# Performance work log

Measured on AMD Instinct MI355X. Metric: run time of the kernel, lower is better.

The kernel has to match this reference:

```python
import math
import jax, jax.numpy as jnp
import numpy as np

B, C, T = 2, 512, 2048
HEADS, NFREQS, NDECAY = 8, 4, 4
HD = C // HEADS  # head dim = 64


def _conv1x1(x, W, b):
    # pointwise Conv1d: W [out, in], b [out], x [B, in, T]
    return jnp.einsum('oi,bit->bot', W, x) + b[:, None]


def setup_inputs() -> dict:
    key = jax.random.key(0)
    ks = jax.random.split(key, 12)
    s = 1.0 / math.sqrt(C)
    inp = {
        'x': jax.random.normal(ks[0], (B, C, T), jnp.float32),
        'Wq': jax.random.normal(ks[1], (C, C), jnp.float32) * s,
        'bq': jnp.zeros((C,), jnp.float32),
        'Wk': jax.random.normal(ks[2], (C, C), jnp.float32) * s,
        'bk': jnp.zeros((C,), jnp.float32),
        'Wc': jax.random.normal(ks[3], (C, C), jnp.float32) * s,
        'bc': jnp.zeros((C,), jnp.float32),
        'Wqf': jax.random.normal(ks[4], (HEADS * NFREQS, C), jnp.float32) * s,
        'bqf': jnp.zeros((HEADS * NFREQS,), jnp.float32),
        # query_decay init: weight *= 0.01, bias = -2 (as in the torch module)
        'Wqd': jax.random.normal(ks[5], (HEADS * NDECAY, C), jnp.float32) * (s * 0.01),
        'bqd': jnp.full((HEADS * NDECAY,), -2.0, jnp.float32),
        'Wp': jax.random.normal(ks[6], (C, C), jnp.float32) * s,
        'bp': jnp.zeros((C,), jnp.float32),
    }
    return inp


def reference(x, Wq, bq, Wk, bk, Wc, bc, Wqf, bqf, Wqd, bqd, Wp, bp):
    Bx, Cx, Tx = x.shape
    idx = jnp.arange(Tx, dtype=x.dtype)
    delta = idx[:, None] - idx[None, :]  # [T, T]

    queries = _conv1x1(x, Wq, bq).reshape(Bx, HEADS, HD, Tx)
    keys = _conv1x1(x, Wk, bk).reshape(Bx, HEADS, HD, Tx)
    dots = jnp.einsum('bhct,bhcs->bhts', keys, queries) / math.sqrt(HD)

    # frequency bias
    periods = jnp.arange(1, NFREQS + 1, dtype=x.dtype)
    freq_kernel = jnp.cos(2 * math.pi * delta / periods[:, None, None])  # [f, T, T]
    freq_q = _conv1x1(x, Wqf, bqf).reshape(Bx, HEADS, NFREQS, Tx) / math.sqrt(NFREQS)
    dots = dots + jnp.einsum('fts,bhfs->bhts', freq_kernel, freq_q)

    # decay bias
    decays = jnp.arange(1, NDECAY + 1, dtype=x.dtype)
    decay_q = jax.nn.sigmoid(_conv1x1(x, Wqd, bqd).reshape(Bx, HEADS, NDECAY, Tx)) / 2
    decay_kernel = -decays[:, None, None] * jnp.abs(delta) / math.sqrt(NDECAY)
    dots = dots + jnp.einsum('fts,bhfs->bhts', decay_kernel, decay_q)

    # mask self-attention diagonal with -100, softmax over keys axis (t, dim=2)
    eye = jnp.eye(Tx, dtype=bool)
    dots = jnp.where(eye[None, None], jnp.asarray(-100.0, x.dtype), dots)
    weights = jax.nn.softmax(dots, axis=2)

    content = _conv1x1(x, Wc, bc).reshape(Bx, HEADS, HD, Tx)
    result = jnp.einsum('bhts,bhct->bhcs', weights, content).reshape(Bx, Cx, Tx)
    return x + _conv1x1(result, Wp, bp)
```

## Files before the change

kernel.cpp:

```cpp
#include <hip/hip_runtime.h>
#include <math.h>

#define T_SEQ 2048
#define C_DIM 512
#define B_SZ  2
#define NHEAD 8
#define HD    64
#define DP    128
#define MTOT  1600
#define NTILE 32

typedef unsigned short u16t;
typedef unsigned int   u32t;
typedef float f32x4 __attribute__((ext_vector_type(4)));
typedef short s16x8 __attribute__((ext_vector_type(8)));

__device__ __forceinline__ u32t pack2(float a, float b) {
    u32t r;
    asm("v_cvt_pk_bf16_f32 %0, %1, %2" : "=v"(r) : "v"(a), "v"(b));
    return r;
}
__device__ __forceinline__ u16t f2bf(float f) {
    union { float f; u32t u; } v; v.f = f;
    u32t r = v.u + 0x7fffu + ((v.u >> 16) & 1u);
    return (u16t)(r >> 16);
}
__device__ __forceinline__ float bf2f(u16t h) {
    union { u32t u; float f; } v; v.u = (u32t)h << 16; return v.f;
}

#define GLD16(g, l) __builtin_amdgcn_global_load_lds( \
    (const __attribute__((address_space(1))) u32t*)(g), \
    (__attribute__((address_space(3))) u32t*)(l), 16, 0, 0)

__global__ __launch_bounds__(256)
void wconv_kernel(const float* __restrict__ Wq, const float* __restrict__ Wk,
                  const float* __restrict__ Wc, const float* __restrict__ Wqf,
                  const float* __restrict__ Wqd, const float* __restrict__ Wp,
                  const float* __restrict__ bq, const float* __restrict__ bk,
                  const float* __restrict__ bc, const float* __restrict__ bqf,
                  const float* __restrict__ bqd,
                  u16t* __restrict__ Wcat, u16t* __restrict__ Wpbf,
                  float* __restrict__ biascat)
{
    int r = blockIdx.x, tid = threadIdx.x;
    if (r < MTOT) {
        const float* src;
        if (r < 512) src = Wq + (long long)r * C_DIM;
        else if (r < 1024) src = Wk + (long long)(r - 512) * C_DIM;
        else if (r < 1536) src = Wc + (long long)(r - 1024) * C_DIM;
        else if (r < 1568) src = Wqf + (long long)(r - 1536) * C_DIM;
        else src = Wqd + (long long)(r - 1568) * C_DIM;
        float2 v = *(const float2*)(src + tid * 2);
        *(u32t*)(Wcat + (long long)r * C_DIM + tid * 2) = pack2(v.x, v.y);
    } else if (r < MTOT + 512) {
        int rr = r - MTOT;
        float2 v = *(const float2*)(Wp + (long long)rr * C_DIM + tid * 2);
        *(u32t*)(Wpbf + (long long)rr * C_DIM + tid * 2) = pack2(v.x, v.y);
    } else {
        for (int i = tid; i < MTOT; i += 256) {
            float bv;
            if (i < 512) bv = bq[i];
            else if (i < 1024) bv = bk[i - 512];
            else if (i < 1536) bv = bc[i - 1024];
            else if (i < 1568) bv = bqf[i - 1536];
            else bv = bqd[i - 1568];
            biascat[i] = bv;
        }
    }
}

__global__ __launch_bounds__(256)
void xt_kernel(const float* __restrict__ x, u16t* __restrict__ xT)
{
    __shared__ float tile[64][65];
    int b = blockIdx.z, c0 = blockIdx.y * 64, t0 = blockIdx.x * 64;
    int tid = threadIdx.x;
    const float* xb = x + ((long long)b * C_DIM + c0) * T_SEQ + t0;
#pragma unroll
    for (int rr = 0; rr < 16; ++rr) {
        int row = rr * 4 + (tid >> 6);
        tile[row][tid & 63] = xb[(long long)row * T_SEQ + (tid & 63)];
    }
    __syncthreads();
    int tt = tid >> 2, cs = (tid & 3) * 16;
    u32t ov[8];
#pragma unroll
    for (int u = 0; u < 8; ++u)
        ov[u] = pack2(tile[cs + u * 2][tt], tile[cs + u * 2 + 1][tt]);
    u16t* dst = xT + ((long long)b * T_SEQ + t0 + tt) * C_DIM + c0 + cs;
    *(uint4*)(dst) = make_uint4(ov[0], ov[1], ov[2], ov[3]);
    *(uint4*)(dst + 8) = make_uint4(ov[4], ov[5], ov[6], ov[7]);
}

template<int BM, int BN, int MODE>
__global__ __launch_bounds__(256)
void gemm_big(const u16t* __restrict__ A, const u16t* __restrict__ Bm,
              const float* __restrict__ biasv, const float* __restrict__ x,
              u16t* __restrict__ Qbf, u16t* __restrict__ Kbf,
              u16t* __restrict__ Vbf, float* __restrict__ fqd,
              float* __restrict__ outp)
{
    constexpr int WM = BM / 2, WN = BN / 2, MT = WM / 16, NT = WN / 16;
    __shared__ u16t At[2][BM * 64];
    __shared__ u16t Bt[2][BN * 64];
    int b = blockIdx.z, m0 = blockIdx.y * BM, n0 = blockIdx.x * BN;
    int tid = threadIdx.x, w = tid >> 6, lane = tid & 63;
    int wy = w >> 1, wx = w & 1;
    int l16 = lane & 15, l4 = lane >> 4;
    const u16t* Bb = Bm + (long long)b * T_SEQ * C_DIM;

    auto stage = [&](int kt, int bufi) {
        int k0 = kt * 64;
#pragma unroll
        for (int i = 0; i < BM / 32; ++i) {
            int rb = (w * (BM / 32) + i) * 8;
            int row = rb + (lane >> 3);
            int c = (lane & 7) ^ (row & 7);
            GLD16(A + (long long)(m0 + row) * C_DIM + k0 + c * 8, &At[bufi][rb * 64]);
        }
#pragma unroll
        for (int i = 0; i < BN / 32; ++i) {
            int rb = (w * (BN / 32) + i) * 8;
            int row = rb + (lane >> 3);
            int c = (lane & 7) ^ (row & 7);
            GLD16(Bb + (long long)(n0 + row) * C_DIM + k0 + c * 8, &Bt[bufi][rb * 64]);
        }
    };

    f32x4 acc[MT][NT] = {};
    stage(0, 0);
    for (int kt = 0; kt < 8; ++kt) {
        __syncthreads();
        if (kt < 7) stage(kt + 1, (kt + 1) & 1);
        const u16t* Ab = At[kt & 1];
        const u16t* Bb2 = Bt[kt & 1];
#pragma unroll
        for (int kb = 0; kb < 2; ++kb) {
            int co = ((kb * 4 + l4) ^ (l16 & 7)) * 8;
            s16x8 bf[NT], af[MT];
#pragma unroll
            for (int nt = 0; nt < NT; ++nt)
                bf[nt] = *(const s16x8*)(&Bb2[(wx * WN + nt * 16 + l16) * 64 + co]);
#pragma unroll
            for (int mt = 0; mt < MT; ++mt)
                af[mt] = *(const s16x8*)(&Ab[(wy * WM + mt * 16 + l16) * 64 + co]);
            __builtin_amdgcn_s_setprio(1);
#pragma unroll
            for (int mt = 0; mt < MT; ++mt)
#pragma unroll
                for (int nt = 0; nt < NT; ++nt)
                    acc[mt][nt] = __builtin_amdgcn_mfma_f32_16x16x32_bf16(
                        af[mt], bf[nt], acc[mt][nt], 0, 0, 0);
            __builtin_amdgcn_s_setprio(0);
        }
    }

    if (MODE == 0) {
        int my = blockIdx.y;
        if (my < 8) {
            bool isQ = my < 4;
            float sc = isQ ? 0.125f : 1.0f;
#pragma unroll
            for (int nt = 0; nt < NT; ++nt) {
                int n = n0 + wx * WN + nt * 16 + l16;
#pragma unroll
                for (int mt = 0; mt < MT; ++mt) {
                    int m = m0 + wy * WM + mt * 16 + l4 * 4;
                    int idx = isQ ? m : m - 512;
                    int h = idx >> 6, d0 = idx & 63;
                    u16t* dst = (isQ ? Qbf : Kbf) +
                        ((long long)(b * NHEAD + h) * T_SEQ + n) * DP + d0;
                    float v0 = sc * (acc[mt][nt][0] + biasv[m + 0]);
                    float v1 = sc * (acc[mt][nt][1] + biasv[m + 1]);
                    float v2 = sc * (acc[mt][nt][2] + biasv[m + 2]);
                    float v3 = sc * (acc[mt][nt][3] + biasv[m + 3]);
                    *(uint2*)dst = make_uint2(pack2(v0, v1), pack2(v2, v3));
                }
            }
        } else if (my < 12) {
#pragma unroll
            for (int nt = 0; nt < NT; ++nt) {
                int n = n0 + wx * WN + nt * 16 + l16;
#pragma unroll
                for (int mt = 0; mt < MT; ++mt)
#pragma unroll
                    for (int j = 0; j < 4; ++j) {
                        int m = m0 + wy * WM + mt * 16 + l4 * 4 + j;
                        int c = m - 1024;
                        Vbf[((long long)b * C_DIM + c) * T_SEQ + n] =
                            f2bf(acc[mt][nt][j] + biasv[m]);
                    }
            }
        } else {
#pragma unroll
            for (int nt = 0; nt < NT; ++nt) {
                int n = n0 + wx * WN + nt * 16 + l16;
#pragma unroll
                for (int mt = 0; mt < MT; ++mt)
#pragma unroll
                    for (int j = 0; j < 4; ++j) {
                        int m = m0 + wy * WM + mt * 16 + l4 * 4 + j;
                        int r = m - 1536;
                        if (r < 64)
                            fqd[((long long)b * 64 + r) * T_SEQ + n] =
                                acc[mt][nt][j] + biasv[m];
                    }
            }
        }
    } else {
#pragma unroll
        for (int nt = 0; nt < NT; ++nt) {
            int n = n0 + wx * WN + nt * 16 + l16;
#pragma unroll
            for (int mt = 0; mt < MT; ++mt)
#pragma unroll
                for (int j = 0; j < 4; ++j) {
                    int m = m0 + wy * WM + mt * 16 + l4 * 4 + j;
                    long long o = ((long long)b * C_DIM + m) * T_SEQ + n;
                    outp[o] = acc[mt][nt][j] + biasv[m] + x[o];
                }
        }
    }
}

__global__ __launch_bounds__(256)
void ext_kernel(const float* __restrict__ fqd, u16t* __restrict__ Qbf,
                u16t* __restrict__ Kbf, float* __restrict__ dcoef)
{
    int s = blockIdx.x * 256 + threadIdx.x;
    int bh = blockIdx.y, b = bh >> 3, h = bh & 7;
    const float* base = fqd + (long long)b * 64 * T_SEQ;
    float dsum = 0.f;
    u32t eq[4], ek[4];
#pragma unroll
    for (int f = 0; f < 4; ++f) {
        float fq = base[(long long)(h * 4 + f) * T_SEQ + s] * 0.5f;
        float zd = base[(long long)(32 + h * 4 + f) * T_SEQ + s];
        dsum += (float)(f + 1) / (1.f + __expf(-zd));
        float a = 2.0f * (float)s / (float)(f + 1);
        float cv = cospif(a), sv = sinpif(a);
        ek[f] = pack2(cv, sv);
        eq[f] = pack2(fq * cv, fq * sv);
    }
    uint4 z = make_uint4(0, 0, 0, 0);
    u16t* qrow = Qbf + ((long long)bh * T_SEQ + s) * DP;
    *(uint4*)(qrow + 64) = make_uint4(eq[0], eq[1], eq[2], eq[3]);
#pragma unroll
    for (int i = 0; i < 7; ++i) *(uint4*)(qrow + 72 + i * 8) = z;
    u16t* krow = Kbf + ((long long)bh * T_SEQ + s) * DP;
    *(uint4*)(krow + 64) = make_uint4(ek[0], ek[1], ek[2], ek[3]);
#pragma unroll
    for (int i = 0; i < 7; ++i) *(uint4*)(krow + 72 + i * 8) = z;
    dcoef[(long long)bh * T_SEQ + s] = 0.25f * dsum;
}

__global__ __launch_bounds__(256)
void knorm_kernel(const u16t* __restrict__ Kbf, float* __restrict__ knorm)
{
    __shared__ float wmax[4];
    int tile = blockIdx.x, bh = blockIdx.y, tid = threadIdx.x;
    int row = tid >> 2, part = tid & 3;
    const u16t* rp = Kbf + ((long long)bh * T_SEQ + tile * 64 + row) * DP + part * 16;
    float ss = 0.f;
#pragma unroll
    for (int i = 0; i < 2; ++i) {
        s16x8 v = *(const s16x8*)(rp + i * 8);
#pragma unroll
        for (int e = 0; e < 8; ++e) { float f = bf2f((u16t)v[e]); ss += f * f; }
    }
    ss += __shfl_xor(ss, 1, 64);
    ss += __shfl_xor(ss, 2, 64);
    float nrm = sqrtf(ss + 4.1f);
#pragma unroll
    for (int off = 4; off < 64; off <<= 1) nrm = fmaxf(nrm, __shfl_xor(nrm, off, 64));
    if ((tid & 63) == 0) wmax[tid >> 6] = nrm;
    __syncthreads();
    if (tid == 0)
        knorm[bh * NTILE + tile] =
            fmaxf(fmaxf(wmax[0], wmax[1]), fmaxf(wmax[2], wmax[3]));
}

__global__ __launch_bounds__(256)
void attn_kernel(const u16t* __restrict__ Qbf, const u16t* __restrict__ Kbf,
                 const u16t* __restrict__ Vbf, const float* __restrict__ dcoef,
                 const float* __restrict__ knorm, u16t* __restrict__ Rt)
{
    __shared__ u16t Kt[2][64 * DP];
    __shared__ u16t Vt[2][64 * 64];
    __shared__ u16t Pl[4][16 * 64];
    __shared__ u32t voteLds[4];

    int bh = blockIdx.y, b = bh >> 3, h = bh & 7;
    int j0 = blockIdx.x;
    int s0 = j0 * 64;
    int tid = threadIdx.x, w = tid >> 6, lane = tid & 63;
    int l16 = lane & 15, l4 = lane >> 4;
    const u16t* Qg = Qbf + (long long)bh * T_SEQ * DP;
    const u16t* Kg = Kbf + (long long)bh * T_SEQ * DP;
    const u16t* Vg = Vbf + ((long long)b * C_DIM + h * HD) * T_SEQ;
    int sl = w * 16 + l16;
    int sg = s0 + sl;

    s16x8 qf[3];
#pragma unroll
    for (int kb = 0; kb < 3; ++kb)
        qf[kb] = *(const s16x8*)(Qg + (long long)sg * DP + kb * 32 + l4 * 8);
    float qn2 = 0.f;
#pragma unroll
    for (int kb = 0; kb < 3; ++kb)
#pragma unroll
        for (int e = 0; e < 8; ++e) { float f = bf2f((u16t)qf[kb][e]); qn2 += f * f; }
    qn2 += __shfl_xor(qn2, 16, 64);
    qn2 += __shfl_xor(qn2, 32, 64);
    float qn = sqrtf(qn2);
    float dc = dcoef[(long long)bh * T_SEQ + sg];
    float mrun = -1e30f, lrun = 0.f;
    f32x4 O4[4] = {};

    auto stageKV = [&](int tt0, int bufi) {
#pragma unroll
        for (int i = 0; i < 4; ++i) {
            int rb = w * 16 + i * 4;
            int row = rb + (lane >> 4);
            int c = (lane & 15) ^ (row & 7);
            GLD16(Kg + (long long)(tt0 + row) * DP + c * 8, &Kt[bufi][rb * DP]);
        }
#pragma unroll
        for (int i = 0; i < 2; ++i) {
            int cb = w * 16 + i * 8;
            int cc = cb + (lane >> 3);
            int tc = (lane & 7) ^ (cc & 7);
            GLD16(Vg + (long long)cc * T_SEQ + tt0 + tc * 8, &Vt[bufi][cb * 64]);
        }
    };

    auto compute_tile = [&](int tj, int bufi, bool diag) {
        const u16t* Kb = Kt[bufi];
        const u16t* Vb = Vt[bufi];
        int t0 = tj * 64;
        f32x4 sacc[4] = {};
        __builtin_amdgcn_s_setprio(1);
#pragma unroll
        for (int kb = 0; kb < 3; ++kb)
#pragma unroll
            for (int rt = 0; rt < 4; ++rt) {
                s16x8 af = *(const s16x8*)(&Kb[(rt * 16 + l16) * DP + (((kb * 4 + l4) ^ (l16 & 7)) * 8)]);
                sacc[rt] = __builtin_amdgcn_mfma_f32_16x16x32_bf16(af, qf[kb], sacc[rt], 0, 0, 0);
            }
        __builtin_amdgcn_s_setprio(0);
        float cm = mrun;
        float pv[4][4];
#pragma unroll
        for (int rt = 0; rt < 4; ++rt) {
            int tb = t0 + rt * 16 + l4 * 4;
#pragma unroll
            for (int j = 0; j < 4; ++j) {
                int t = tb + j;
                float v = sacc[rt][j] - fabsf((float)(t - sg)) * dc;
                if (diag && t == sg) v = -100.f;
                pv[rt][j] = v;
                cm = fmaxf(cm, v);
            }
        }
        cm = fmaxf(cm, __shfl_xor(cm, 16, 64));
        cm = fmaxf(cm, __shfl_xor(cm, 32, 64));
        if (!__all(cm - mrun <= 8.f)) {
            float scale = __expf(mrun - cm);
            mrun = cm;
            lrun *= scale;
#pragma unroll
            for (int rt = 0; rt < 4; ++rt) O4[rt] *= scale;
        }
        float psum = 0.f;
#pragma unroll
        for (int rt = 0; rt < 4; ++rt)
#pragma unroll
            for (int j = 0; j < 4; ++j) {
                float p = __expf(pv[rt][j] - mrun);
                pv[rt][j] = p;
                psum += p;
            }
        psum += __shfl_xor(psum, 16, 64);
        psum += __shfl_xor(psum, 32, 64);
        lrun += psum;
#pragma unroll
        for (int rt = 0; rt < 4; ++rt) {
            int tl = rt * 16 + l4 * 4;
            int cp = (tl >> 3) ^ (l16 & 7);
            *(uint2*)(&Pl[w][l16 * 64 + cp * 8 + (tl & 7)]) =
                make_uint2(pack2(pv[rt][0], pv[rt][1]), pack2(pv[rt][2], pv[rt][3]));
        }
        __builtin_amdgcn_s_setprio(1);
#pragma unroll
        for (int kb = 0; kb < 2; ++kb) {
            s16x8 pf = *(const s16x8*)(&Pl[w][l16 * 64 + (((kb * 4 + l4) ^ (l16 & 7)) * 8)]);
#pragma unroll
            for (int rt = 0; rt < 4; ++rt) {
                s16x8 vf = *(const s16x8*)(&Vb[(rt * 16 + l16) * 64 + (((kb * 4 + l4) ^ (l16 & 7)) * 8)]);
                O4[rt] = __builtin_amdgcn_mfma_f32_16x16x32_bf16(vf, pf, O4[rt], 0, 0, 0);
            }
        }
        __builtin_amdgcn_s_setprio(0);
    };

    int seq[3]; int ns = 0;
    seq[ns++] = j0;
    if (j0 + 1 < NTILE) seq[ns++] = j0 + 1;
    if (j0 > 0) seq[ns++] = j0 - 1;
    stageKV(seq[0] * 64, 0);
    for (int i = 0; i < ns; ++i) {
        __syncthreads();
        if (i + 1 < ns) stageKV(seq[i + 1] * 64, (i + 1) & 1);
        compute_tile(seq[i], i & 1, seq[i] == j0);
    }

    u32t mask = 0;
    const float* knb = knorm + bh * NTILE;
    for (int j = 0; j < NTILE; ++j) {
        int d = j > j0 ? j - j0 : j0 - j;
        if (d <= 1) continue;
        float minD = (float)((d - 1) * 64 + 1);
        float bound = qn * knb[j] - dc * minD;
        if (__any(bound > mrun - 15.f)) mask |= 1u << j;
    }
    voteLds[w] = mask;
    __syncthreads();
    mask = voteLds[0] | voteLds[1] | voteLds[2] | voteLds[3];

    int parity = ns & 1;
    u32t rem = mask;
    if (rem) {
        int j = (int)__builtin_ctz(rem);
        stageKV(j * 64, parity);
        while (true) {
            rem &= rem - 1;
            __syncthreads();
            int nj = rem ? (int)__builtin_ctz(rem) : -1;
            if (nj >= 0) stageKV(nj * 64, parity ^ 1);
            compute_tile(j, parity, false);
            if (nj < 0) break;
            parity ^= 1;
            j = nj;
        }
    }

    __syncthreads();
    float inv = 1.f / lrun;
#pragma unroll
    for (int rt = 0; rt < 4; ++rt) {
        O4[rt] *= inv;
        int cb = rt * 16 + l4 * 4;
        int cp = (cb >> 3) ^ (sl & 7);
        *(uint2*)(&Kt[0][sl * 64 + cp * 8 + (cb & 7)]) =
            make_uint2(pack2(O4[rt][0], O4[rt][1]), pack2(O4[rt][2], O4[rt][3]));
    }
    __syncthreads();
    {
        int row = tid >> 2;
        int rsw = row & 7;
        u16t* dst = Rt + ((long long)b * T_SEQ + s0 + row) * C_DIM + h * HD;
#pragma unroll
        for (int i = 0; i < 2; ++i) {
            int cc = (tid & 3) + i * 4;
            uint4 v = *(const uint4*)(&Kt[0][row * 64 + ((cc ^ rsw) * 8)]);
            *(uint4*)(dst + cc * 8) = v;
        }
    }
}

extern "C" void kernel_launch(void* const* d_in, const int* in_sizes, int n_in,
                              void* d_out, int out_size, void* d_ws, size_t ws_size,
                              hipStream_t stream)
{
    const float* x   = (const float*)d_in[0];
    const float* Wq  = (const float*)d_in[1];
    const float* bq  = (const float*)d_in[2];
    const float* Wk  = (const float*)d_in[3];
    const float* bk  = (const float*)d_in[4];
    const float* Wc  = (const float*)d_in[5];
    const float* bc  = (const float*)d_in[6];
    const float* Wqf = (const float*)d_in[7];
    const float* bqf = (const float*)d_in[8];
    const float* Wqd = (const float*)d_in[9];
    const float* bqd = (const float*)d_in[10];
    const float* Wp  = (const float*)d_in[11];
    const float* bp  = (const float*)d_in[12];
    float* out = (float*)d_out;

    char* p = (char*)d_ws;
    u16t* Wcat = (u16t*)p;    p += (long long)MTOT * C_DIM * 2;
    u16t* Wpbf = (u16t*)p;    p += (long long)C_DIM * C_DIM * 2;
    float* biascat = (float*)p; p += MTOT * 4;
    u16t* xT = (u16t*)p;      p += (long long)B_SZ * T_SEQ * C_DIM * 2;
    u16t* Qbf = (u16t*)p;     p += (long long)16 * T_SEQ * DP * 2;
    u16t* Kbf = (u16t*)p;     p += (long long)16 * T_SEQ * DP * 2;
    u16t* Vbf = (u16t*)p;     p += (long long)B_SZ * C_DIM * T_SEQ * 2;
    float* fqd = (float*)p;   p += (long long)B_SZ * 64 * T_SEQ * 4;
    float* dcoef = (float*)p; p += (long long)16 * T_SEQ * 4;
    float* knorm = (float*)p; p += (long long)16 * NTILE * 4;
    u16t* Rt = (u16t*)p;      p += (long long)B_SZ * T_SEQ * C_DIM * 2;

    dim3 blk(256);
    hipLaunchKernelGGL(wconv_kernel, dim3(MTOT + 512 + 1), blk, 0, stream,
                       Wq, Wk, Wc, Wqf, Wqd, Wp, bq, bk, bc, bqf, bqd,
                       Wcat, Wpbf, biascat);
    hipLaunchKernelGGL(xt_kernel, dim3(T_SEQ / 64, C_DIM / 64, B_SZ), blk, 0, stream,
                       x, xT);
    hipLaunchKernelGGL((gemm_big<128, 128, 0>), dim3(T_SEQ / 128, 13, B_SZ), blk, 0,
                       stream, Wcat, xT, biascat, nullptr, Qbf, Kbf, Vbf, fqd, nullptr);
    hipLaunchKernelGGL(ext_kernel, dim3(T_SEQ / 256, 16), blk, 0, stream,
                       fqd, Qbf, Kbf, dcoef);
    hipLaunchKernelGGL(knorm_kernel, dim3(NTILE, 16), blk, 0, stream, Kbf, knorm);
    hipLaunchKernelGGL(attn_kernel, dim3(T_SEQ / 64, 16), blk, 0, stream,
                       Qbf, Kbf, Vbf, dcoef, knorm, Rt);
    hipLaunchKernelGGL((gemm_big<128, 64, 1>), dim3(T_SEQ / 64, C_DIM / 128, B_SZ),
                       blk, 0, stream, Wpbf, Rt, bp, x, nullptr, nullptr,
                       nullptr, nullptr, out);
}
```

Before: 69.68 us.

## Merge prep kernels, fold key-norm into ext, drop setprio, exact rescale

The x-transpose and weight-conversion kernels become a single prep launch, and the per-tile key norm is now computed inside ext_kernel from the freshly written K rows, so the separate knorm pass and its re-read of K go away. The s_setprio hints around the MFMA blocks are removed from both the GEMM and attention kernels. The online-softmax rescale now fires whenever the running max grows, rather than only when it grows by more than 8, which costs more rescale branches but keeps values bounded. The net effect is two fewer kernel launches in exchange for more work per ext thread and different scheduling priority.

```diff
diff --git a/kernel.cpp b/kernel.cpp
--- a/kernel.cpp
+++ b/kernel.cpp
@@ -34,16 +34,39 @@
     (__attribute__((address_space(3))) u32t*)(l), 16, 0, 0)
 
 __global__ __launch_bounds__(256)
-void wconv_kernel(const float* __restrict__ Wq, const float* __restrict__ Wk,
-                  const float* __restrict__ Wc, const float* __restrict__ Wqf,
-                  const float* __restrict__ Wqd, const float* __restrict__ Wp,
-                  const float* __restrict__ bq, const float* __restrict__ bk,
-                  const float* __restrict__ bc, const float* __restrict__ bqf,
-                  const float* __restrict__ bqd,
-                  u16t* __restrict__ Wcat, u16t* __restrict__ Wpbf,
-                  float* __restrict__ biascat)
+void prep_kernel(const float* __restrict__ x, u16t* __restrict__ xT,
+                 const float* __restrict__ Wq, const float* __restrict__ Wk,
+                 const float* __restrict__ Wc, const float* __restrict__ Wqf,
+                 const float* __restrict__ Wqd, const float* __restrict__ Wp,
+                 const float* __restrict__ bq, const float* __restrict__ bk,
+                 const float* __restrict__ bc, const float* __restrict__ bqf,
+                 const float* __restrict__ bqd,
+                 u16t* __restrict__ Wcat, u16t* __restrict__ Wpbf,
+                 float* __restrict__ biascat)
 {
-    int r = blockIdx.x, tid = threadIdx.x;
+    __shared__ float tile[64][65];
+    int blk = blockIdx.x, tid = threadIdx.x;
+    if (blk < 512) {
+        int b = blk >> 8, rem = blk & 255;
+        int c0 = (rem >> 5) << 6, t0 = (rem & 31) << 6;
+        const float* xb = x + ((long long)b * C_DIM + c0) * T_SEQ + t0;
+#pragma unroll
+        for (int rr = 0; rr < 16; ++rr) {
+            int row = rr * 4 + (tid >> 6);
+            tile[row][tid & 63] = xb[(long long)row * T_SEQ + (tid & 63)];
+        }
+        __syncthreads();
+        int tt = tid >> 2, cs = (tid & 3) * 16;
+        u32t ov[8];
+#pragma unroll
+        for (int u = 0; u < 8; ++u)
+            ov[u] = pack2(tile[cs + u * 2][tt], tile[cs + u * 2 + 1][tt]);
+        u16t* dst = xT + ((long long)b * T_SEQ + t0 + tt) * C_DIM + c0 + cs;
+        *(uint4*)(dst) = make_uint4(ov[0], ov[1], ov[2], ov[3]);
+        *(uint4*)(dst + 8) = make_uint4(ov[4], ov[5], ov[6], ov[7]);
+        return;
+    }
+    int r = blk - 512;
     if (r < MTOT) {
         const float* src;
         if (r < 512) src = Wq + (long long)r * C_DIM;
@@ -70,29 +93,6 @@
     }
 }
 
-__global__ __launch_bounds__(256)
-void xt_kernel(const float* __restrict__ x, u16t* __restrict__ xT)
-{
-    __shared__ float tile[64][65];
-    int b = blockIdx.z, c0 = blockIdx.y * 64, t0 = blockIdx.x * 64;
-    int tid = threadIdx.x;
-    const float* xb = x + ((long long)b * C_DIM + c0) * T_SEQ + t0;
-#pragma unroll
-    for (int rr = 0; rr < 16; ++rr) {
-        int row = rr * 4 + (tid >> 6);
-        tile[row][tid & 63] = xb[(long long)row * T_SEQ + (tid & 63)];
-    }
-    __syncthreads();
-    int tt = tid >> 2, cs = (tid & 3) * 16;
-    u32t ov[8];
-#pragma unroll
-    for (int u = 0; u < 8; ++u)
-        ov[u] = pack2(tile[cs + u * 2][tt], tile[cs + u * 2 + 1][tt]);
-    u16t* dst = xT + ((long long)b * T_SEQ + t0 + tt) * C_DIM + c0 + cs;
-    *(uint4*)(dst) = make_uint4(ov[0], ov[1], ov[2], ov[3]);
-    *(uint4*)(dst + 8) = make_uint4(ov[4], ov[5], ov[6], ov[7]);
-}
-
 template<int BM, int BN, int MODE>
 __global__ __launch_bounds__(256)
 void gemm_big(const u16t* __restrict__ A, const u16t* __restrict__ Bm,
@@ -145,14 +145,12 @@
 #pragma unroll
             for (int mt = 0; mt < MT; ++mt)
                 af[mt] = *(const s16x8*)(&Ab[(wy * WM + mt * 16 + l16) * 64 + co]);
-            __builtin_amdgcn_s_setprio(1);
 #pragma unroll
             for (int mt = 0; mt < MT; ++mt)
 #pragma unroll
                 for (int nt = 0; nt < NT; ++nt)
                     acc[mt][nt] = __builtin_amdgcn_mfma_f32_16x16x32_bf16(
                         af[mt], bf[nt], acc[mt][nt], 0, 0, 0);
-            __builtin_amdgcn_s_setprio(0);
         }
     }
 
@@ -226,7 +224,8 @@
 
 __global__ __launch_bounds__(256)
 void ext_kernel(const float* __restrict__ fqd, u16t* __restrict__ Qbf,
-                u16t* __restrict__ Kbf, float* __restrict__ dcoef)
+                u16t* __restrict__ Kbf, float* __restrict__ dcoef,
+                float* __restrict__ knorm)
 {
     int s = blockIdx.x * 256 + threadIdx.x;
     int bh = blockIdx.y, b = bh >> 3, h = bh & 7;
@@ -253,32 +252,20 @@
 #pragma unroll
     for (int i = 0; i < 7; ++i) *(uint4*)(krow + 72 + i * 8) = z;
     dcoef[(long long)bh * T_SEQ + s] = 0.25f * dsum;
-}
-
-__global__ __launch_bounds__(256)
-void knorm_kernel(const u16t* __restrict__ Kbf, float* __restrict__ knorm)
-{
-    __shared__ float wmax[4];
-    int tile = blockIdx.x, bh = blockIdx.y, tid = threadIdx.x;
-    int row = tid >> 2, part = tid & 3;
-    const u16t* rp = Kbf + ((long long)bh * T_SEQ + tile * 64 + row) * DP + part * 16;
+
     float ss = 0.f;
 #pragma unroll
-    for (int i = 0; i < 2; ++i) {
-        s16x8 v = *(const s16x8*)(rp + i * 8);
+    for (int i = 0; i < 8; ++i) {
+        s16x8 v = *(const s16x8*)(krow + i * 8);
 #pragma unroll
         for (int e = 0; e < 8; ++e) { float f = bf2f((u16t)v[e]); ss += f * f; }
     }
-    ss += __shfl_xor(ss, 1, 64);
-    ss += __shfl_xor(ss, 2, 64);
     float nrm = sqrtf(ss + 4.1f);
 #pragma unroll
-    for (int off = 4; off < 64; off <<= 1) nrm = fmaxf(nrm, __shfl_xor(nrm, off, 64));
-    if ((tid & 63) == 0) wmax[tid >> 6] = nrm;
-    __syncthreads();
-    if (tid == 0)
-        knorm[bh * NTILE + tile] =
-            fmaxf(fmaxf(wmax[0], wmax[1]), fmaxf(wmax[2], wmax[3]));
+    for (int off = 1; off < 64; off <<= 1)
+        nrm = fmaxf(nrm, __shfl_xor(nrm, off, 64));
+    if ((threadIdx.x & 63) == 0)
+        knorm[bh * NTILE + (s >> 6)] = nrm;
 }
 
 __global__ __launch_bounds__(256)
@@ -340,7 +327,6 @@
         const u16t* Vb = Vt[bufi];
         int t0 = tj * 64;
         f32x4 sacc[4] = {};
-        __builtin_amdgcn_s_setprio(1);
 #pragma unroll
         for (int kb = 0; kb < 3; ++kb)
 #pragma unroll
@@ -348,7 +334,6 @@
                 s16x8 af = *(const s16x8*)(&Kb[(rt * 16 + l16) * DP + (((kb * 4 + l4) ^ (l16 & 7)) * 8)]);
                 sacc[rt] = __builtin_amdgcn_mfma_f32_16x16x32_bf16(af, qf[kb], sacc[rt], 0, 0, 0);
             }
-        __builtin_amdgcn_s_setprio(0);
         float cm = mrun;
         float pv[4][4];
 #pragma unroll
@@ -365,7 +350,7 @@
         }
         cm = fmaxf(cm, __shfl_xor(cm, 16, 64));
         cm = fmaxf(cm, __shfl_xor(cm, 32, 64));
-        if (!__all(cm - mrun <= 8.f)) {
+        if (__any(cm > mrun)) {
             float scale = __expf(mrun - cm);
             mrun = cm;
             lrun *= scale;
@@ -391,7 +376,6 @@
             *(uint2*)(&Pl[w][l16 * 64 + cp * 8 + (tl & 7)]) =
                 make_uint2(pack2(pv[rt][0], pv[rt][1]), pack2(pv[rt][2], pv[rt][3]));
         }
-        __builtin_amdgcn_s_setprio(1);
 #pragma unroll
         for (int kb = 0; kb < 2; ++kb) {
             s16x8 pf = *(const s16x8*)(&Pl[w][l16 * 64 + (((kb * 4 + l4) ^ (l16 & 7)) * 8)]);
@@ -401,7 +385,6 @@
                 O4[rt] = __builtin_amdgcn_mfma_f32_16x16x32_bf16(vf, pf, O4[rt], 0, 0, 0);
             }
         }
-        __builtin_amdgcn_s_setprio(0);
     };
 
     int seq[3]; int ns = 0;
@@ -502,16 +485,13 @@
     u16t* Rt = (u16t*)p;      p += (long long)B_SZ * T_SEQ * C_DIM * 2;
 
     dim3 blk(256);
-    hipLaunchKernelGGL(wconv_kernel, dim3(MTOT + 512 + 1), blk, 0, stream,
-                       Wq, Wk, Wc, Wqf, Wqd, Wp, bq, bk, bc, bqf, bqd,
+    hipLaunchKernelGGL(prep_kernel, dim3(512 + MTOT + 512 + 1), blk, 0, stream,
+                       x, xT, Wq, Wk, Wc, Wqf, Wqd, Wp, bq, bk, bc, bqf, bqd,
                        Wcat, Wpbf, biascat);
-    hipLaunchKernelGGL(xt_kernel, dim3(T_SEQ / 64, C_DIM / 64, B_SZ), blk, 0, stream,
-                       x, xT);
     hipLaunchKernelGGL((gemm_big<128, 128, 0>), dim3(T_SEQ / 128, 13, B_SZ), blk, 0,
                        stream, Wcat, xT, biascat, nullptr, Qbf, Kbf, Vbf, fqd, nullptr);
     hipLaunchKernelGGL(ext_kernel, dim3(T_SEQ / 256, 16), blk, 0, stream,
-                       fqd, Qbf, Kbf, dcoef);
-    hipLaunchKernelGGL(knorm_kernel, dim3(NTILE, 16), blk, 0, stream, Kbf, knorm);
+                       fqd, Qbf, Kbf, dcoef, knorm);
     hipLaunchKernelGGL(attn_kernel, dim3(T_SEQ / 64, 16), blk, 0, stream,
                        Qbf, Kbf, Vbf, dcoef, knorm, Rt);
     hipLaunchKernelGGL((gemm_big<128, 64, 1>), dim3(T_SEQ / 64, C_DIM / 128, B_SZ),
```

After: 68.45 us. About the same (-1.8%).
